# Performance work log

Hardware: AMD Instinct MI355X
Metric: run time of the kernel (lower is better)

Reference implementation:

```python
import jax, jax.numpy as jnp
import numpy as np

DIM, HEADS, WIN, SHIFT = 384, 12, 7, 3
H, W = 56, 56
HEAD_DIM = DIM // HEADS
SCALE = HEAD_DIM ** -0.5
N = WIN * WIN


def _relative_index():
    coords = np.stack(np.meshgrid(np.arange(WIN), np.arange(WIN), indexing='ij')).reshape(2, -1)
    rel = (coords[:, :, None] - coords[:, None, :]).transpose(1, 2, 0)
    rel[:, :, 0] += WIN - 1
    rel[:, :, 1] += WIN - 1
    rel[:, :, 0] *= 2 * WIN - 1
    return rel.sum(-1)  # [N, N] int


def _attn_mask():
    img = np.zeros((H, W), dtype=np.float32)
    cnt = 0
    sls = (slice(0, -WIN), slice(-WIN, -SHIFT), slice(-SHIFT, None))
    for hs in sls:
        for ws in sls:
            img[hs, ws] = cnt
            cnt += 1
    m = img.reshape(H // WIN, WIN, W // WIN, WIN).transpose(0, 2, 1, 3).reshape(-1, N)  # [nw, N]
    diff = m[:, None, :] - m[:, :, None]  # [nw, N, N]
    return np.where(diff != 0, -10000.0, 0.0).astype(np.float32)

REL_IDX = jnp.asarray(_relative_index())
MASK = jnp.asarray(_attn_mask())  # [nw, N, N]


def _layernorm(x, w, b):
    mu = x.mean(-1, keepdims=True)
    var = ((x - mu) ** 2).mean(-1, keepdims=True)
    return (x - mu) * jax.lax.rsqrt(var + 1e-5) * w + b


def _window_partition(x):  # [B,H,W,C] -> [B*nw, N, C]
    B, _, _, C = x.shape
    x = x.reshape(B, H // WIN, WIN, W // WIN, WIN, C)
    x = x.transpose(0, 1, 3, 2, 4, 5)
    return x.reshape(-1, N, C)


def _window_reverse(w, B):  # [B*nw, N, C] -> [B,H,W,C]
    C = w.shape[-1]
    x = w.reshape(B, H // WIN, W // WIN, WIN, WIN, C)
    x = x.transpose(0, 1, 3, 2, 4, 5)
    return x.reshape(B, H, W, C)


def setup_inputs() -> dict:
    key = jax.random.key(0)
    ks = jax.random.split(key, 12)
    s = DIM ** -0.5
    return {
        'x': jax.random.normal(ks[0], (32, H * W, DIM), jnp.float32),
        'qkv_w': jax.random.normal(ks[1], (DIM, 3 * DIM), jnp.float32) * s,  # stored [in,out]
        'qkv_b': jnp.zeros((3 * DIM,), jnp.float32),
        'proj_w': jax.random.normal(ks[2], (DIM, DIM), jnp.float32) * s,
        'proj_b': jnp.zeros((DIM,), jnp.float32),
        'rel_bias': jax.random.normal(ks[3], ((2 * WIN - 1) ** 2, HEADS), jnp.float32) * 0.02,
        'norm1_w': jnp.ones((DIM,), jnp.float32),
        'norm1_b': jnp.zeros((DIM,), jnp.float32),
        'norm2_w': jnp.ones((DIM,), jnp.float32),
        'norm2_b': jnp.zeros((DIM,), jnp.float32),
        'mlp_w1': jax.random.normal(ks[4], (DIM, 4 * DIM), jnp.float32) * s,
        'mlp_b1': jnp.zeros((4 * DIM,), jnp.float32),
        'mlp_w2': jax.random.normal(ks[5], (4 * DIM, DIM), jnp.float32) * (4 * DIM) ** -0.5,
        'mlp_b2': jnp.zeros((DIM,), jnp.float32),
    }


def _forward(x, qkv_w, qkv_b, proj_w, proj_b, rel_bias, norm1_w, norm1_b,
             norm2_w, norm2_b, mlp_w1, mlp_b1, mlp_w2, mlp_b2):
    B, L, C = x.shape
    residual = x
    h = _layernorm(x, norm1_w, norm1_b).reshape(B, H, W, C)
    h = jnp.roll(h, (-SHIFT, -SHIFT), axis=(1, 2))
    wx = _window_partition(h)  # [B_, N, C]
    B_ = wx.shape[0]

    qkv = (wx @ qkv_w + qkv_b).reshape(B_, N, 3, HEADS, HEAD_DIM)
    q, k, v = qkv[:, :, 0], qkv[:, :, 1], qkv[:, :, 2]  # [B_, N, h, d]
    attn = jnp.einsum('bnhd,bmhd->bhnm', q * SCALE, k)  # [B_, h, N, N]
    rb = rel_bias[REL_IDX.reshape(-1)].reshape(N, N, HEADS).transpose(2, 0, 1)
    attn = attn + rb[None]
    nw = MASK.shape[0]
    attn = attn.reshape(B_ // nw, nw, HEADS, N, N) + MASK[None, :, None]
    attn = jax.nn.softmax(attn.reshape(B_, HEADS, N, N), axis=-1)
    out = jnp.einsum('bhnm,bmhd->bnhd', attn, v).reshape(B_, N, C)
    out = out @ proj_w + proj_b

    h = _window_reverse(out, B)
    h = jnp.roll(h, (SHIFT, SHIFT), axis=(1, 2))
    x = h.reshape(B, L, C) + residual

    m = _layernorm(x, norm2_w, norm2_b)
    m = jax.nn.gelu(m @ mlp_w1 + mlp_b1, approximate=False) @ mlp_w2 + mlp_b2
    return x + m


def reference(x, qkv_w, qkv_b, proj_w, proj_b, rel_bias, norm1_w, norm1_b,
              norm2_w, norm2_b, mlp_w1, mlp_b1, mlp_w2, mlp_b2):
    return _forward(x, qkv_w, qkv_b, proj_w, proj_b, rel_bias, norm1_w, norm1_b,
                    norm2_w, norm2_b, mlp_w1, mlp_b1, mlp_w2, mlp_b2)
```

## Files before the change

kernel.cpp:

```cpp
#include <hip/hip_runtime.h>
#include <hip/hip_bf16.h>

typedef unsigned short u16;
typedef __bf16 bf16x8 __attribute__((ext_vector_type(8)));
typedef float f32x4 __attribute__((ext_vector_type(4)));

#define HH 56
#define WW 56
#define DIM 384
#define NTOK 100352
#define NWIN 2048
#define NN 49

__device__ __forceinline__ u16 f2bf(float f) {
    __hip_bfloat16 h = __float2bfloat16(f);
    return *reinterpret_cast<u16*>(&h);
}
__device__ __forceinline__ float bf2f(u16 u) {
    union { unsigned int i; float f; } c; c.i = ((unsigned int)u) << 16; return c.f;
}

__device__ __forceinline__ float fast_gelu(float x) {
    float au = fabsf(x) * 0.70710678118654752f;
    float t = __builtin_amdgcn_rcpf(fmaf(0.3275911f, au, 1.0f));
    float p = fmaf(t, 1.061405429f, -1.453152027f);
    p = fmaf(t, p, 1.421413741f);
    p = fmaf(t, p, -0.284496736f);
    p = fmaf(t, p, 0.254829592f);
    p = p * t;
    float e = __expf(-au * au);
    float erfau = fmaf(-p, e, 1.0f);
    float erfx = __builtin_copysignf(erfau, x);
    return 0.5f * x * (1.0f + erfx);
}

#define GLD_LDS(gp, lp) __builtin_amdgcn_global_load_lds( \
    (const __attribute__((address_space(1))) void*)(gp), \
    (__attribute__((address_space(3))) void*)(lp), 16, 0, 0)

__global__ void castT(const float* __restrict__ in, u16* __restrict__ out, int K, int N) {
    int i = blockIdx.x * 256 + threadIdx.x;
    if (i < N * K) {
        int n = i / K, kk = i - n * K;
        out[i] = f2bf(in[(size_t)kk * N + n]);
    }
}

__global__ void bias_kernel(const float* __restrict__ rel_bias, float* __restrict__ Tb) {
    int ty = blockIdx.x / 12, h = blockIdx.x - ty * 12;
    for (int i = threadIdx.x; i < 4096; i += 256) {
        int q = i >> 6, kk = i & 63;
        float v;
        if (kk >= 49) v = -1e30f;
        else if (q >= 49) v = 0.f;
        else {
            int rn = q / 7, cn = q - rn * 7;
            int rm = kk / 7, cm = kk - rm * 7;
            float rb = rel_bias[((rn - rm + 6) * 13 + (cn - cm + 6)) * 12 + h];
            int h0 = (ty >> 1) ? 49 : 0;
            int w0 = (ty & 1) ? 49 : 0;
            int hn = h0 + rn, hm = h0 + rm, wn = w0 + cn, wm = w0 + cm;
            int regn = (hn < 49 ? 0 : (hn < 53 ? 1 : 2)) * 3 + (wn < 49 ? 0 : (wn < 53 ? 1 : 2));
            int regm = (hm < 49 ? 0 : (hm < 53 ? 1 : 2)) * 3 + (wm < 49 ? 0 : (wm < 53 ? 1 : 2));
            v = rb + ((regn == regm) ? 0.f : -10000.f);
        }
        Tb[(size_t)blockIdx.x * 4096 + i] = v;
    }
}

template<bool WIN_MAP>
__global__ __launch_bounds__(256) void ln_kernel(
    const float* __restrict__ x, const float* __restrict__ w, const float* __restrict__ b,
    u16* __restrict__ out)
{
    int token = blockIdx.x * 4 + (threadIdx.x >> 6);
    int lane = threadIdx.x & 63;
    const float* row = x + (size_t)token * DIM;
    float v[6]; float sum = 0.f, sq = 0.f;
#pragma unroll
    for (int j = 0; j < 3; j++) {
        float2 p = *(const float2*)(row + lane * 2 + j * 128);
        v[2*j] = p.x; v[2*j+1] = p.y;
        sum += p.x + p.y; sq += p.x * p.x + p.y * p.y;
    }
#pragma unroll
    for (int off = 32; off; off >>= 1) { sum += __shfl_xor(sum, off); sq += __shfl_xor(sq, off); }
    float mu = sum * (1.f / DIM);
    float rstd = rsqrtf(sq * (1.f / DIM) - mu * mu + 1e-5f);
    size_t obase;
    if (WIN_MAP) {
        int b_ = token / 3136, hw = token - b_ * 3136;
        int h = hw / WW, wc_ = hw - h * WW;
        int hr = h - 3; if (hr < 0) hr += HH;
        int wr = wc_ - 3; if (wr < 0) wr += WW;
        int win = b_ * 64 + (hr / 7) * 8 + (wr / 7);
        int n = (hr % 7) * 7 + (wr % 7);
        obase = ((size_t)win * NN + n) * DIM;
    } else {
        obase = (size_t)token * DIM;
    }
#pragma unroll
    for (int j = 0; j < 3; j++) {
        int c = lane * 2 + j * 128;
        float a0 = (v[2*j]   - mu) * rstd * w[c]   + b[c];
        float a1 = (v[2*j+1] - mu) * rstd * w[c+1] + b[c+1];
        unsigned int pair = (unsigned int)f2bf(a0) | ((unsigned int)f2bf(a1) << 16);
        *(unsigned int*)(out + obase + c) = pair;
    }
}

template<int EPI, bool REV>
__global__ __launch_bounds__(512, 4) void gemm_kernel(
    const u16* __restrict__ A, const u16* __restrict__ Bt,
    const float* __restrict__ bias, const float* __restrict__ resid,
    void* __restrict__ outp, int N, int K, int BNT)
{
    __shared__ u16 sA[2][8192];
    __shared__ u16 sB[2][4096];
    const int tid = threadIdx.x;
    const int lane = tid & 63;
    const int wave = tid >> 6;
    const int wr = wave >> 1, wc = wave & 1;

    const int q8 = gridDim.x >> 3;
    int wg = (blockIdx.x & 7) * q8 + (blockIdx.x >> 3);
    if (REV) wg = gridDim.x - 1 - wg;
    const int bm = wg / BNT, bn = wg - bm * BNT;

    f32x4 acc[4][4] = {};

    const int r0 = tid >> 2;
    const int sg = (tid & 3) ^ (r0 & 3) ^ ((r0 >> 2) & 3);
    const u16* Arow0 = A + (size_t)(bm * 256 + r0) * K + sg * 8;
    const u16* Arow1 = Arow0 + (size_t)128 * K;
    const u16* Brow0 = Bt + (size_t)(bn * 128 + r0) * K + sg * 8;

    const int nt = K >> 5;

#define STAGE(t, buf) do { \
        int kt_ = (t) * 32; \
        GLD_LDS(Arow0 + kt_, &sA[buf][wave * 512]); \
        GLD_LDS(Arow1 + kt_, &sA[buf][4096 + wave * 512]); \
        GLD_LDS(Brow0 + kt_, &sB[buf][wave * 512]); \
    } while (0)

    STAGE(0, 0); STAGE(1, 1);

    const int l15 = lane & 15, g = lane >> 4;
    const int ssr = (g ^ (l15 & 3) ^ ((l15 >> 2) & 3)) * 8;

    for (int t = 0; t < nt; t++) {
        const int bsel = t & 1;
        if (t + 1 < nt) asm volatile("s_waitcnt vmcnt(3)" ::: "memory");
        else            asm volatile("s_waitcnt vmcnt(0)" ::: "memory");
        __builtin_amdgcn_s_barrier();
        __builtin_amdgcn_sched_barrier(0);
        bf16x8 af[4], bfr[4];
#pragma unroll
        for (int m = 0; m < 4; m++) {
            int row = wr * 64 + m * 16 + l15;
            af[m] = *(const bf16x8*)&sA[bsel][row * 32 + ssr];
        }
#pragma unroll
        for (int n = 0; n < 4; n++) {
            int row = wc * 64 + n * 16 + l15;
            bfr[n] = *(const bf16x8*)&sB[bsel][row * 32 + ssr];
        }
        asm volatile("s_waitcnt lgkmcnt(0)" ::: "memory");
        __builtin_amdgcn_sched_barrier(0);
        __builtin_amdgcn_s_barrier();
        __builtin_amdgcn_sched_barrier(0);
        if (t + 2 < nt) STAGE(t + 2, bsel);
#pragma unroll
        for (int m = 0; m < 4; m++)
#pragma unroll
            for (int n = 0; n < 4; n++)
                acc[m][n] = __builtin_amdgcn_mfma_f32_16x16x32_bf16(af[m], bfr[n], acc[m][n], 0, 0, 0);
    }
#undef STAGE

    const int col0 = bn * 128 + wc * 64 + l15;
    float bias4[4];
#pragma unroll
    for (int nn = 0; nn < 4; nn++) bias4[nn] = bias[col0 + nn * 16];

#pragma unroll
    for (int m = 0; m < 4; m++) {
#pragma unroll
        for (int r = 0; r < 4; r++) {
            int row = bm * 256 + wr * 64 + m * 16 + (g << 2) + r;
            size_t obase;
            if (EPI == 1) {
                int win = row / NN, n = row - win * NN;
                int b_ = win >> 6, wi = win & 63;
                int hr = (wi >> 3) * 7 + n / 7;
                int wcl = (wi & 7) * 7 + n % 7;
                int hf = hr + 3; if (hf >= HH) hf -= HH;
                int wf = wcl + 3; if (wf >= WW) wf -= WW;
                obase = ((size_t)b_ * 3136 + hf * WW + wf) * DIM;
            } else {
                obase = (size_t)row * N;
            }
#pragma unroll
            for (int nn = 0; nn < 4; nn++) {
                int col = col0 + nn * 16;
                float val = acc[m][nn][r] + bias4[nn];
                if (EPI == 0) {
                    ((u16*)outp)[obase + col] = f2bf(val);
                } else if (EPI == 1) {
                    ((float*)outp)[obase + col] = val + resid[obase + col];
                } else if (EPI == 2) {
                    ((u16*)outp)[obase + col] = f2bf(fast_gelu(val));
                } else {
                    ((float*)outp)[obase + col] = val + resid[obase + col];
                }
            }
        }
    }
}

__global__ __launch_bounds__(256) void attn_kernel(
    const u16* __restrict__ qkv, const float* __restrict__ Tb,
    u16* __restrict__ attn_out)
{
    __shared__ u16 smem[4][6912];
    const int win = blockIdx.x;
    const int wave = threadIdx.x >> 6;
    const int lane = threadIdx.x & 63;
    const int head = blockIdx.y * 4 + wave;
    const int l15 = lane & 15, g = lane >> 4;

    u16* Vt = smem[wave];
    u16* P  = Vt + 2304;

    const u16* qkvw = qkv + (size_t)win * NN * 1152 + head * 32;

    {
        int m = lane;
        bool real = m < NN;
        const u16* vrow = qkvw + (size_t)(real ? m : 0) * 1152 + 768;
        int4 z = {0,0,0,0};
        int4 c0 = real ? *(const int4*)(vrow)      : z;
        int4 c1 = real ? *(const int4*)(vrow + 8)  : z;
        int4 c2 = real ? *(const int4*)(vrow + 16) : z;
        int4 c3 = real ? *(const int4*)(vrow + 24) : z;
        u16 vals[32];
        *(int4*)&vals[0]  = c0; *(int4*)&vals[8]  = c1;
        *(int4*)&vals[16] = c2; *(int4*)&vals[24] = c3;
#pragma unroll
        for (int d = 0; d < 32; d++) Vt[d * 72 + m] = vals[d];
    }

    bf16x8 kf[4], qf[4];
#pragma unroll
    for (int t = 0; t < 4; t++) {
        int row = t * 16 + l15; if (row > 48) row = 48;
        const u16* base = qkvw + (size_t)row * 1152 + g * 8;
        kf[t] = *(const bf16x8*)(base + 384);
        qf[t] = *(const bf16x8*)(base);
    }
    f32x4 s[4][4];
#pragma unroll
    for (int mt = 0; mt < 4; mt++)
#pragma unroll
        for (int nt = 0; nt < 4; nt++) {
            f32x4 zero = {};
            s[mt][nt] = __builtin_amdgcn_mfma_f32_16x16x32_bf16(kf[mt], qf[nt], zero, 0, 0, 0);
        }

    const int wi = win & 63;
    const int ty = (((wi >> 3) == 7) ? 2 : 0) + (((wi & 7) == 7) ? 1 : 0);
    const float* tbb = Tb + (((size_t)ty * 12 + head) << 12);
    const float SCALE = 0.17677669529663687f;
#pragma unroll
    for (int nt = 0; nt < 4; nt++) {
        int q = nt * 16 + l15;
        const float* trow = tbb + q * 64 + g * 4;
        f32x4 b[4];
#pragma unroll
        for (int mt = 0; mt < 4; mt++) b[mt] = *(const f32x4*)(trow + mt * 16);
        float mx = -3e38f;
#pragma unroll
        for (int mt = 0; mt < 4; mt++)
#pragma unroll
            for (int r = 0; r < 4; r++) {
                float v = s[mt][nt][r] * SCALE + b[mt][r];
                s[mt][nt][r] = v;
                mx = fmaxf(mx, v);
            }
        mx = fmaxf(mx, __shfl_xor(mx, 16));
        mx = fmaxf(mx, __shfl_xor(mx, 32));
        float sum = 0.f;
#pragma unroll
        for (int mt = 0; mt < 4; mt++)
#pragma unroll
            for (int r = 0; r < 4; r++) {
                float e = __expf(s[mt][nt][r] - mx);
                s[mt][nt][r] = e;
                sum += e;
            }
        sum += __shfl_xor(sum, 16);
        sum += __shfl_xor(sum, 32);
        float inv = 1.f / sum;
#pragma unroll
        for (int mt = 0; mt < 4; mt++) {
            unsigned int p01 = (unsigned int)f2bf(s[mt][nt][0] * inv) | ((unsigned int)f2bf(s[mt][nt][1] * inv) << 16);
            unsigned int p23 = (unsigned int)f2bf(s[mt][nt][2] * inv) | ((unsigned int)f2bf(s[mt][nt][3] * inv) << 16);
            uint2 pk; pk.x = p01; pk.y = p23;
            *(uint2*)&P[(unsigned)q * 72 + mt * 16 + g * 4] = pk;
        }
    }

    bf16x8 vf[2][2];
#pragma unroll
    for (int ks = 0; ks < 2; ks++)
#pragma unroll
        for (int dt = 0; dt < 2; dt++)
            vf[ks][dt] = *(const bf16x8*)&Vt[(dt * 16 + l15) * 72 + ks * 32 + g * 8];

    f32x4 o[4][2] = {};
#pragma unroll
    for (int nt = 0; nt < 4; nt++) {
        bf16x8 pf0 = *(const bf16x8*)&P[(nt * 16 + l15) * 72 + g * 8];
        bf16x8 pf1 = *(const bf16x8*)&P[(nt * 16 + l15) * 72 + 32 + g * 8];
#pragma unroll
        for (int dt = 0; dt < 2; dt++) {
            o[nt][dt] = __builtin_amdgcn_mfma_f32_16x16x32_bf16(pf0, vf[0][dt], o[nt][dt], 0, 0, 0);
            o[nt][dt] = __builtin_amdgcn_mfma_f32_16x16x32_bf16(pf1, vf[1][dt], o[nt][dt], 0, 0, 0);
        }
    }

#pragma unroll
    for (int nt = 0; nt < 4; nt++)
#pragma unroll
        for (int r = 0; r < 4; r++) {
            int q = nt * 16 + 4 * g + r;
            if (q < NN) {
                size_t ob = ((size_t)win * NN + q) * DIM + head * 32;
                attn_out[ob + l15]      = f2bf(o[nt][0][r]);
                attn_out[ob + 16 + l15] = f2bf(o[nt][1][r]);
            }
        }
}

extern "C" void kernel_launch(void* const* d_in, const int* in_sizes, int n_in,
                              void* d_out, int out_size, void* d_ws, size_t ws_size,
                              hipStream_t stream)
{
    const float* x      = (const float*)d_in[0];
    const float* qkv_w  = (const float*)d_in[1];
    const float* qkv_b  = (const float*)d_in[2];
    const float* proj_w = (const float*)d_in[3];
    const float* proj_b = (const float*)d_in[4];
    const float* rel_b  = (const float*)d_in[5];
    const float* n1w    = (const float*)d_in[6];
    const float* n1b    = (const float*)d_in[7];
    const float* n2w    = (const float*)d_in[8];
    const float* n2b    = (const float*)d_in[9];
    const float* w1     = (const float*)d_in[10];
    const float* b1     = (const float*)d_in[11];
    const float* w2     = (const float*)d_in[12];
    const float* b2     = (const float*)d_in[13];

    char* ws = (char*)d_ws;
    u16* hidden  = (u16*)(ws);
    u16* qkvbuf  = hidden;
    float* Tb    = (float*)(ws + 231211008);
    u16* wxbuf   = (u16*)(ws + 308281344);
    u16* qkv_wt  = (u16*)(ws + 385351680);
    u16* proj_wt = (u16*)(ws + 386236416);
    u16* w1t     = (u16*)(ws + 386531328);
    u16* w2t     = (u16*)(ws + 387710976);

    castT<<<(1152*384 + 255) / 256, 256, 0, stream>>>(qkv_w, qkv_wt, 384, 1152);
    castT<<<(384*384  + 255) / 256, 256, 0, stream>>>(proj_w, proj_wt, 384, 384);
    castT<<<(384*1536 + 255) / 256, 256, 0, stream>>>(w1, w1t, 384, 1536);
    castT<<<(1536*384 + 255) / 256, 256, 0, stream>>>(w2, w2t, 1536, 384);
    bias_kernel<<<48, 256, 0, stream>>>(rel_b, Tb);

    ln_kernel<true><<<NTOK / 4, 256, 0, stream>>>(x, n1w, n1b, wxbuf);
    gemm_kernel<0, true><<<392 * 9, 512, 0, stream>>>(wxbuf, qkv_wt, qkv_b, nullptr, qkvbuf, 1152, 384, 9);
    attn_kernel<<<dim3(NWIN, 3), 256, 0, stream>>>(qkvbuf, Tb, wxbuf);
    gemm_kernel<1, true><<<392 * 3, 512, 0, stream>>>(wxbuf, proj_wt, proj_b, x, d_out, 384, 384, 3);
    ln_kernel<false><<<NTOK / 4, 256, 0, stream>>>((const float*)d_out, n2w, n2b, wxbuf);
    gemm_kernel<2, true><<<392 * 12, 512, 0, stream>>>(wxbuf, w1t, b1, nullptr, hidden, 1536, 384, 12);
    gemm_kernel<3, false><<<392 * 3, 512, 0, stream>>>(hidden, w2t, b2, (const float*)d_out, d_out, 384, 1536, 3);
}
```

Baseline: 880.2 us.

## Make GEMM kernel process multiple tiles per block with cross-tile prefetch

```diff
diff --git a/kernel.cpp b/kernel.cpp
--- a/kernel.cpp
+++ b/kernel.cpp
@@ -109,11 +109,11 @@
     }
 }
 
-template<int EPI, bool REV>
+template<int EPI, bool REV, int TPB>
 __global__ __launch_bounds__(512, 4) void gemm_kernel(
     const u16* __restrict__ A, const u16* __restrict__ Bt,
     const float* __restrict__ bias, const float* __restrict__ resid,
-    void* __restrict__ outp, int N, int K, int BNT)
+    void* __restrict__ outp, int N, int K, int BNT, int NT_TOT)
 {
     __shared__ u16 sA[2][8192];
     __shared__ u16 sB[2][4096];
@@ -122,101 +122,117 @@
     const int wave = tid >> 6;
     const int wr = wave >> 1, wc = wave & 1;
 
-    const int q8 = gridDim.x >> 3;
-    int wg = (blockIdx.x & 7) * q8 + (blockIdx.x >> 3);
-    if (REV) wg = gridDim.x - 1 - wg;
-    const int bm = wg / BNT, bn = wg - bm * BNT;
-
-    f32x4 acc[4][4] = {};
+    const int q8t = NT_TOT >> 3;
+    const int chunk = blockIdx.x & 7;
+    const int base = (blockIdx.x >> 3) * TPB;
 
     const int r0 = tid >> 2;
     const int sg = (tid & 3) ^ (r0 & 3) ^ ((r0 >> 2) & 3);
-    const u16* Arow0 = A + (size_t)(bm * 256 + r0) * K + sg * 8;
-    const u16* Arow1 = Arow0 + (size_t)128 * K;
-    const u16* Brow0 = Bt + (size_t)(bn * 128 + r0) * K + sg * 8;
-
     const int nt = K >> 5;
-
-#define STAGE(t, buf) do { \
-        int kt_ = (t) * 32; \
-        GLD_LDS(Arow0 + kt_, &sA[buf][wave * 512]); \
-        GLD_LDS(Arow1 + kt_, &sA[buf][4096 + wave * 512]); \
-        GLD_LDS(Brow0 + kt_, &sB[buf][wave * 512]); \
-    } while (0)
-
-    STAGE(0, 0); STAGE(1, 1);
-
     const int l15 = lane & 15, g = lane >> 4;
     const int ssr = (g ^ (l15 & 3) ^ ((l15 >> 2) & 3)) * 8;
 
-    for (int t = 0; t < nt; t++) {
-        const int bsel = t & 1;
-        if (t + 1 < nt) asm volatile("s_waitcnt vmcnt(3)" ::: "memory");
-        else            asm volatile("s_waitcnt vmcnt(0)" ::: "memory");
-        __builtin_amdgcn_s_barrier();
-        __builtin_amdgcn_sched_barrier(0);
-        bf16x8 af[4], bfr[4];
+#define DECODE(j, oA0, oA1, oB0, obm, obn) do { \
+        int wg_ = chunk * q8t + base + (j); \
+        if (REV) wg_ = NT_TOT - 1 - wg_; \
+        obm = wg_ / BNT; obn = wg_ - obm * BNT; \
+        oA0 = A + (size_t)(obm * 256 + r0) * K + sg * 8; \
+        oA1 = oA0 + (size_t)128 * K; \
+        oB0 = Bt + (size_t)(obn * 128 + r0) * K + sg * 8; \
+    } while (0)
+
+#define STAGEP(t, buf, pA0, pA1, pB0) do { \
+        int kt_ = (t) * 32; \
+        GLD_LDS(pA0 + kt_, &sA[buf][wave * 512]); \
+        GLD_LDS(pA1 + kt_, &sA[buf][4096 + wave * 512]); \
+        GLD_LDS(pB0 + kt_, &sB[buf][wave * 512]); \
+    } while (0)
+
+    const u16 *cA0, *cA1, *cB0;
+    int cbm, cbn;
+    DECODE(0, cA0, cA1, cB0, cbm, cbn);
+    const u16 *nA0 = cA0, *nA1 = cA1, *nB0 = cB0;
+    int nbm = cbm, nbn = cbn;
+
+    STAGEP(0, 0, cA0, cA1, cB0);
+    STAGEP(1, 1, cA0, cA1, cB0);
+
+    for (int j = 0; j < TPB; j++) {
+        const bool hasNext = (j + 1 < TPB);
+        if (hasNext) DECODE(j + 1, nA0, nA1, nB0, nbm, nbn);
+        f32x4 acc[4][4] = {};
+        for (int t = 0; t < nt; t++) {
+            const int bsel = t & 1;
+            if (t + 1 < nt || hasNext) asm volatile("s_waitcnt vmcnt(3)" ::: "memory");
+            else                       asm volatile("s_waitcnt vmcnt(0)" ::: "memory");
+            __builtin_amdgcn_s_barrier();
+            __builtin_amdgcn_sched_barrier(0);
+            bf16x8 af[4], bfr[4];
+#pragma unroll
+            for (int m = 0; m < 4; m++) {
+                int row = wr * 64 + m * 16 + l15;
+                af[m] = *(const bf16x8*)&sA[bsel][row * 32 + ssr];
+            }
+#pragma unroll
+            for (int n = 0; n < 4; n++) {
+                int row = wc * 64 + n * 16 + l15;
+                bfr[n] = *(const bf16x8*)&sB[bsel][row * 32 + ssr];
+            }
+            asm volatile("s_waitcnt lgkmcnt(0)" ::: "memory");
+            __builtin_amdgcn_sched_barrier(0);
+            __builtin_amdgcn_s_barrier();
+            __builtin_amdgcn_sched_barrier(0);
+            if (t + 2 < nt)   STAGEP(t + 2, bsel, cA0, cA1, cB0);
+            else if (hasNext) STAGEP(t + 2 - nt, bsel, nA0, nA1, nB0);
+#pragma unroll
+            for (int m = 0; m < 4; m++)
+#pragma unroll
+                for (int n = 0; n < 4; n++)
+                    acc[m][n] = __builtin_amdgcn_mfma_f32_16x16x32_bf16(af[m], bfr[n], acc[m][n], 0, 0, 0);
+        }
+
+        const int col0 = cbn * 128 + wc * 64 + l15;
+        float bias4[4];
+#pragma unroll
+        for (int nn = 0; nn < 4; nn++) bias4[nn] = bias[col0 + nn * 16];
+
 #pragma unroll
         for (int m = 0; m < 4; m++) {
-            int row = wr * 64 + m * 16 + l15;
-            af[m] = *(const bf16x8*)&sA[bsel][row * 32 + ssr];
-        }
-#pragma unroll
-        for (int n = 0; n < 4; n++) {
-            int row = wc * 64 + n * 16 + l15;
-            bfr[n] = *(const bf16x8*)&sB[bsel][row * 32 + ssr];
-        }
-        asm volatile("s_waitcnt lgkmcnt(0)" ::: "memory");
-        __builtin_amdgcn_sched_barrier(0);
-        __builtin_amdgcn_s_barrier();
-        __builtin_amdgcn_sched_barrier(0);
-        if (t + 2 < nt) STAGE(t + 2, bsel);
-#pragma unroll
-        for (int m = 0; m < 4; m++)
-#pragma unroll
-            for (int n = 0; n < 4; n++)
-                acc[m][n] = __builtin_amdgcn_mfma_f32_16x16x32_bf16(af[m], bfr[n], acc[m][n], 0, 0, 0);
-    }
-#undef STAGE
-
-    const int col0 = bn * 128 + wc * 64 + l15;
-    float bias4[4];
-#pragma unroll
-    for (int nn = 0; nn < 4; nn++) bias4[nn] = bias[col0 + nn * 16];
-
-#pragma unroll
-    for (int m = 0; m < 4; m++) {
-#pragma unroll
-        for (int r = 0; r < 4; r++) {
-            int row = bm * 256 + wr * 64 + m * 16 + (g << 2) + r;
-            size_t obase;
-            if (EPI == 1) {
-                int win = row / NN, n = row - win * NN;
-                int b_ = win >> 6, wi = win & 63;
-                int hr = (wi >> 3) * 7 + n / 7;
-                int wcl = (wi & 7) * 7 + n % 7;
-                int hf = hr + 3; if (hf >= HH) hf -= HH;
-                int wf = wcl + 3; if (wf >= WW) wf -= WW;
-                obase = ((size_t)b_ * 3136 + hf * WW + wf) * DIM;
-            } else {
-                obase = (size_t)row * N;
-            }
-#pragma unroll
-            for (int nn = 0; nn < 4; nn++) {
-                int col = col0 + nn * 16;
-                float val = acc[m][nn][r] + bias4[nn];
-                if (EPI == 0) {
-                    ((u16*)outp)[obase + col] = f2bf(val);
-                } else if (EPI == 1) {
-                    ((float*)outp)[obase + col] = val + resid[obase + col];
-                } else if (EPI == 2) {
-                    ((u16*)outp)[obase + col] = f2bf(fast_gelu(val));
+#pragma unroll
+            for (int r = 0; r < 4; r++) {
+                int row = cbm * 256 + wr * 64 + m * 16 + (g << 2) + r;
+                size_t obase;
+                if (EPI == 1) {
+                    int win = row / NN, n = row - win * NN;
+                    int b_ = win >> 6, wi = win & 63;
+                    int hr = (wi >> 3) * 7 + n / 7;
+                    int wcl = (wi & 7) * 7 + n % 7;
+                    int hf = hr + 3; if (hf >= HH) hf -= HH;
+                    int wf = wcl + 3; if (wf >= WW) wf -= WW;
+                    obase = ((size_t)b_ * 3136 + hf * WW + wf) * DIM;
                 } else {
-                    ((float*)outp)[obase + col] = val + resid[obase + col];
+                    obase = (size_t)row * N;
                 }
-            }
-        }
-    }
+#pragma unroll
+                for (int nn = 0; nn < 4; nn++) {
+                    int col = col0 + nn * 16;
+                    float val = acc[m][nn][r] + bias4[nn];
+                    if (EPI == 0) {
+                        ((u16*)outp)[obase + col] = f2bf(val);
+                    } else if (EPI == 1) {
+                        ((float*)outp)[obase + col] = val + resid[obase + col];
+                    } else if (EPI == 2) {
+                        ((u16*)outp)[obase + col] = f2bf(fast_gelu(val));
+                    } else {
+                        ((float*)outp)[obase + col] = val + resid[obase + col];
+                    }
+                }
+            }
+        }
+        cA0 = nA0; cA1 = nA1; cB0 = nB0; cbm = nbm; cbn = nbn;
+    }
+#undef STAGEP
+#undef DECODE
 }
 
 __global__ __launch_bounds__(256) void attn_kernel(
@@ -379,10 +395,10 @@
     bias_kernel<<<48, 256, 0, stream>>>(rel_b, Tb);
 
     ln_kernel<true><<<NTOK / 4, 256, 0, stream>>>(x, n1w, n1b, wxbuf);
-    gemm_kernel<0, true><<<392 * 9, 512, 0, stream>>>(wxbuf, qkv_wt, qkv_b, nullptr, qkvbuf, 1152, 384, 9);
+    gemm_kernel<0, true, 3><<<1176, 512, 0, stream>>>(wxbuf, qkv_wt, qkv_b, nullptr, qkvbuf, 1152, 384, 9, 3528);
     attn_kernel<<<dim3(NWIN, 3), 256, 0, stream>>>(qkvbuf, Tb, wxbuf);
-    gemm_kernel<1, true><<<392 * 3, 512, 0, stream>>>(wxbuf, proj_wt, proj_b, x, d_out, 384, 384, 3);
+    gemm_kernel<1, true, 1><<<1176, 512, 0, stream>>>(wxbuf, proj_wt, proj_b, x, d_out, 384, 384, 3, 1176);
     ln_kernel<false><<<NTOK / 4, 256, 0, stream>>>((const float*)d_out, n2w, n2b, wxbuf);
-    gemm_kernel<2, true><<<392 * 12, 512, 0, stream>>>(wxbuf, w1t, b1, nullptr, hidden, 1536, 384, 12);
-    gemm_kernel<3, false><<<392 * 3, 512, 0, stream>>>(hidden, w2t, b2, (const float*)d_out, d_out, 384, 1536, 3);
-}
+    gemm_kernel<2, true, 6><<<784, 512, 0, stream>>>(wxbuf, w1t, b1, nullptr, hidden, 1536, 384, 12, 4704);
+    gemm_kernel<3, false, 1><<<1176, 512, 0, stream>>>(hidden, w2t, b2, (const float*)d_out, d_out, 384, 1536, 3, 1176);
+}
```

After: 926.8 us. 1.05x slower.
